# Optimization experiments

Measured on AMD Instinct MI355X. Metric: run time of the kernel, lower is better.

Reference implementation:

```python
import jax, jax.numpy as jnp
import numpy as np

EPS = 1e-5

def layernorm(x, w, b):
    mu = jnp.mean(x, axis=-1, keepdims=True)
    var = jnp.mean((x - mu) ** 2, axis=-1, keepdims=True)
    return (x - mu) / jnp.sqrt(var + EPS) * w + b

def setup_inputs() -> dict:
    key = jax.random.key(0)
    ks = jax.random.split(key, 20)
    N, E, G = 50000, 800000, 512
    IN, OUT, TXT, MAN = 128, 128, 768, 14
    d = {
        "x": jax.random.normal(ks[0], (N, IN), jnp.float32),
        "edge_index": jax.random.randint(ks[1], (2, E), 0, N),
        "batch": jnp.sort(jax.random.randint(ks[2], (N,), 0, G)),
        "batch_size": G,
        "text_embedding": jax.random.normal(ks[3], (G, TXT), jnp.float32),
        "features_embedding": jax.random.normal(ks[4], (G, MAN), jnp.float32),
        # params
        "ln_proj_w": jnp.ones((IN,)), "ln_proj_b": jnp.zeros((IN,)),
        "W_l": jax.random.normal(ks[5], (IN, OUT)) / np.sqrt(IN),
        "b_l": jnp.zeros((OUT,)),
        "W_r": jax.random.normal(ks[6], (IN, OUT)) / np.sqrt(IN),
        "ln_conv_w": jnp.ones((OUT,)), "ln_conv_b": jnp.zeros((OUT,)),
        "gate_w": jax.random.normal(ks[7], (OUT, 1)) / np.sqrt(OUT),
        "gate_b": jnp.zeros((1,)),
        "graph_weight": jnp.asarray(1.0, jnp.float32),
        "msg_W": jax.random.normal(ks[8], (TXT, OUT)) / np.sqrt(TXT),
        "msg_b": jnp.zeros((OUT,)),
        "feat_W": jax.random.normal(ks[9], (MAN, OUT)) / np.sqrt(MAN),
        "feat_b": jnp.zeros((OUT,)),
        "mixed_w": jnp.ones((3 * OUT,)), "mixed_b": jnp.zeros((3 * OUT,)),
        "fc1_W": jax.random.normal(ks[10], (3 * OUT, 1)) / np.sqrt(3 * OUT),
        "fc1_b": jnp.zeros((1,)),
    }
    return d

def reference(x, edge_index, batch, batch_size, text_embedding, features_embedding,
              ln_proj_w, ln_proj_b, W_l, b_l, W_r, ln_conv_w, ln_conv_b,
              gate_w, gate_b, graph_weight, msg_W, msg_b, feat_W, feat_b,
              mixed_w, mixed_b, fc1_W, fc1_b):
    N = x.shape[0]
    src, dst = edge_index[0], edge_index[1]
    # project_norm
    h = layernorm(x, ln_proj_w, ln_proj_b)
    # GraphSAGE (SAGEConv, mean aggregation): out = mean_j(h_j) @ W_l + b + h @ W_r
    msgs = h[src]                                   # [E, IN] gather
    agg = jax.ops.segment_sum(msgs, dst, num_segments=N)
    deg = jax.ops.segment_sum(jnp.ones((src.shape[0],), h.dtype), dst, num_segments=N)
    mean_nb = agg / jnp.maximum(deg, 1.0)[:, None]
    h = mean_nb @ W_l + b_l + h @ W_r
    # layernorm + gelu (HomogeneousGraphConvolution)
    h = jax.nn.gelu(layernorm(h, ln_conv_w, ln_conv_b), approximate=False)
    # AttentionalAggregation: scatter-softmax over `batch`
    gate = (h @ gate_w + gate_b)[:, 0]              # [N]
    seg_max = jax.ops.segment_max(gate, batch, num_segments=batch_size)
    seg_max = jnp.where(jnp.isfinite(seg_max), seg_max, 0.0)
    e = jnp.exp(gate - seg_max[batch])
    denom = jax.ops.segment_sum(e, batch, num_segments=batch_size)
    attn = (e / denom[batch])[:, None]              # [N,1]
    graph_embedding = jax.ops.segment_sum(attn * h, batch, num_segments=batch_size)
    # dropout is identity in eval mode
    weighted = graph_weight * graph_embedding
    msg_emb = jax.nn.gelu(text_embedding @ msg_W + msg_b, approximate=False)
    feat_emb = jax.nn.gelu(features_embedding @ feat_W + feat_b, approximate=False)
    emb = jnp.concatenate([weighted, msg_emb, feat_emb], axis=1)
    emb = layernorm(emb, mixed_w, mixed_b)
    logits = emb @ fc1_W + fc1_b
    return (logits, graph_embedding, attn)
```

## Files before the change

### kernel.cpp

```cpp
#include <hip/hip_runtime.h>


typedef unsigned short ushort_t;
typedef __attribute__((ext_vector_type(8))) short bf16x8;
typedef __attribute__((ext_vector_type(4))) float floatx4;

__device__ __forceinline__ float b2f(ushort_t u) {
    union { unsigned int i; float f; } v; v.i = ((unsigned int)u) << 16; return v.f;
}
__device__ __forceinline__ ushort_t f2b(float f) {
    union { float f; unsigned int i; } v; v.f = f;
    unsigned int x = v.i;
    return (ushort_t)((x + 0x7FFFu + ((x >> 16) & 1u)) >> 16);
}
__device__ __forceinline__ float gelu_f(float x) {
    return 0.5f * x * (1.0f + erff(x * 0.70710678118654752440f));
}
__device__ __forceinline__ float waveReduceSum(float v) {
#pragma unroll
    for (int o = 32; o; o >>= 1) v += __shfl_xor(v, o, 64);
    return v;
}
__device__ __forceinline__ int waveReduceSumI(int v) {
#pragma unroll
    for (int o = 32; o; o >>= 1) v += __shfl_xor(v, o, 64);
    return v;
}
__device__ __forceinline__ float waveReduceMax(float v) {
#pragma unroll
    for (int o = 32; o; o >>= 1) v = fmaxf(v, __shfl_xor(v, o, 64));
    return v;
}
__device__ __forceinline__ int lowerBound(const int* __restrict__ a, int n, int v) {
    int lo = 0, hi = n;
    while (lo < hi) { int mid = (lo + hi) >> 1; if (a[mid] < v) lo = mid + 1; else hi = mid; }
    return lo;
}
__device__ __forceinline__ void acc8(float* a, const bf16x8& r) {
    a[0] += b2f((ushort_t)r[0]); a[1] += b2f((ushort_t)r[1]);
    a[2] += b2f((ushort_t)r[2]); a[3] += b2f((ushort_t)r[3]);
    a[4] += b2f((ushort_t)r[4]); a[5] += b2f((ushort_t)r[5]);
    a[6] += b2f((ushort_t)r[6]); a[7] += b2f((ushort_t)r[7]);
}

__global__ void __launch_bounds__(256) k_cpl(
    const float* __restrict__ x, const float* __restrict__ w, const float* __restrict__ b,
    const float* __restrict__ Wl, const float* __restrict__ Wr,
    const int* __restrict__ ei, int* __restrict__ deg,
    ushort_t* __restrict__ Wt, ushort_t* __restrict__ hb, int N, int E, int ebc) {
    int bid = blockIdx.x;
    if (bid < ebc) {
        int i0 = (bid * 256 + threadIdx.x) * 8;
        const int* dstp = ei + E;
        if (i0 + 7 < E) {
            int4 a = *(const int4*)(dstp + i0);
            int4 c = *(const int4*)(dstp + i0 + 4);
            atomicAdd(&deg[a.x], 1); atomicAdd(&deg[a.y], 1);
            atomicAdd(&deg[a.z], 1); atomicAdd(&deg[a.w], 1);
            atomicAdd(&deg[c.x], 1); atomicAdd(&deg[c.y], 1);
            atomicAdd(&deg[c.z], 1); atomicAdd(&deg[c.w], 1);
        } else {
            int e1 = min(i0 + 8, E);
            for (int i = i0; i < e1; i++) atomicAdd(&deg[dstp[i]], 1);
        }
        return;
    }
    bid -= ebc;
    if (bid < 128) {
        int id = bid * 256 + threadIdx.x;
        int n = id >> 8, k = id & 255;
        float v = (k < 128) ? Wl[k * 128 + n] : Wr[(k - 128) * 128 + n];
        Wt[n * 256 + k] = f2b(v);
        return;
    }
    int lb = bid - 128;
    int row  = lb * 4 + (threadIdx.x >> 6);
    int lane = threadIdx.x & 63;
    if (row >= N) return;
    size_t base = (size_t)row * 128;
    float2 xv = ((const float2*)(x + base))[lane];
    float v0 = xv.x, v1 = xv.y;
    float s  = waveReduceSum(v0 + v1);
    float s2 = waveReduceSum(v0 * v0 + v1 * v1);
    float mu = s * (1.0f / 128.0f);
    float var = s2 * (1.0f / 128.0f) - mu * mu;
    float rstd = 1.0f / sqrtf(var + 1e-5f);
    int d = lane * 2;
    ushort2 ov;
    ov.x = f2b((v0 - mu) * rstd * w[d]     + b[d]);
    ov.y = f2b((v1 - mu) * rstd * w[d + 1] + b[d + 1]);
    ((ushort2*)(hb + base))[lane] = ov;
}

__global__ void __launch_bounds__(256) k_cursor3(
    const int* __restrict__ deg, int* __restrict__ cursor, int* __restrict__ wcur, int N) {
    int c = blockIdx.x, t = threadIdx.x;
    __shared__ int sb[256];
    __shared__ int cw[4];
    int lim = c << 8;
    int part = 0;
    for (int j = t; j < lim; j += 256) part += deg[j];
    part = waveReduceSumI(part);
    int lane = t & 63, wv = t >> 6;
    if (lane == 0) cw[wv] = part;
    int i = (c << 8) + t;
    int v = (i < N) ? deg[i] : 0;
    sb[t] = v;
    __syncthreads();
    for (int o = 1; o < 256; o <<= 1) {
        int a = (t >= o) ? sb[t - o] : 0;
        __syncthreads();
        sb[t] += a;
        __syncthreads();
    }
    int coff = cw[0] + cw[1] + cw[2] + cw[3];
    if (i < N) {
        int cv = sb[t] - v + coff;
        cursor[i] = cv;
        wcur[i]   = cv;
    }
}

__global__ void __launch_bounds__(256) k_place(
    const int* __restrict__ ei, int* __restrict__ wcur, int* __restrict__ nbr, int E) {
    int i0 = (blockIdx.x * 256 + threadIdx.x) * 8;
    if (i0 + 7 < E) {
        int4 s0 = *(const int4*)(ei + i0);
        int4 s1 = *(const int4*)(ei + i0 + 4);
        int4 d0 = *(const int4*)(ei + E + i0);
        int4 d1 = *(const int4*)(ei + E + i0 + 4);
        int p0 = atomicAdd(&wcur[d0.x], 1);
        int p1 = atomicAdd(&wcur[d0.y], 1);
        int p2 = atomicAdd(&wcur[d0.z], 1);
        int p3 = atomicAdd(&wcur[d0.w], 1);
        int p4 = atomicAdd(&wcur[d1.x], 1);
        int p5 = atomicAdd(&wcur[d1.y], 1);
        int p6 = atomicAdd(&wcur[d1.z], 1);
        int p7 = atomicAdd(&wcur[d1.w], 1);
        nbr[p0] = s0.x; nbr[p1] = s0.y; nbr[p2] = s0.z; nbr[p3] = s0.w;
        nbr[p4] = s1.x; nbr[p5] = s1.y; nbr[p6] = s1.z; nbr[p7] = s1.w;
    } else {
        int e1 = min(i0 + 8, E);
        for (int i = i0; i < e1; i++) {
            int s = ei[i], d = ei[E + i];
            nbr[atomicAdd(&wcur[d], 1)] = s;
        }
    }
}

__global__ void __launch_bounds__(256) k_aggemm(
    const ushort_t* __restrict__ hb, const ushort_t* __restrict__ Wt,
    const float* __restrict__ bl, const float* __restrict__ lnw,
    const float* __restrict__ lnb, const float* __restrict__ gw,
    const float* __restrict__ gb, const int* __restrict__ deg,
    const int* __restrict__ cursor, const int* __restrict__ nbr,
    ushort_t* __restrict__ h3b, float* __restrict__ gate, int N) {
    __shared__ ushort_t A[16][264];
    __shared__ float H2[16][132];
    int t = threadIdx.x;
    int row0 = blockIdx.x * 16;
    int w = t >> 6, l = t & 63;
    int sub = l >> 4, li = l & 15;
    {
        int r = w * 4 + sub;
        int node = row0 + r; if (node >= N) node = N - 1;
        bf16x8 hv = *(const bf16x8*)(hb + (size_t)node * 128 + li * 8);
        *(bf16x8*)&A[r][128 + li * 8] = hv;
        int dg = deg[node];
        int st = cursor[node];
        float a[8] = {0.f, 0.f, 0.f, 0.f, 0.f, 0.f, 0.f, 0.f};
        int j = 0;
        for (; j + 8 <= dg; j += 8) {
            int s0 = nbr[st + j],     s1 = nbr[st + j + 1];
            int s2 = nbr[st + j + 2], s3 = nbr[st + j + 3];
            int s4 = nbr[st + j + 4], s5 = nbr[st + j + 5];
            int s6 = nbr[st + j + 6], s7 = nbr[st + j + 7];
            bf16x8 r0 = *(const bf16x8*)(hb + (size_t)s0 * 128 + li * 8);
            bf16x8 r1 = *(const bf16x8*)(hb + (size_t)s1 * 128 + li * 8);
            bf16x8 r2 = *(const bf16x8*)(hb + (size_t)s2 * 128 + li * 8);
            bf16x8 r3 = *(const bf16x8*)(hb + (size_t)s3 * 128 + li * 8);
            bf16x8 r4 = *(const bf16x8*)(hb + (size_t)s4 * 128 + li * 8);
            bf16x8 r5 = *(const bf16x8*)(hb + (size_t)s5 * 128 + li * 8);
            bf16x8 r6 = *(const bf16x8*)(hb + (size_t)s6 * 128 + li * 8);
            bf16x8 r7 = *(const bf16x8*)(hb + (size_t)s7 * 128 + li * 8);
            acc8(a, r0); acc8(a, r1); acc8(a, r2); acc8(a, r3);
            acc8(a, r4); acc8(a, r5); acc8(a, r6); acc8(a, r7);
        }
        for (; j + 4 <= dg; j += 4) {
            int s0 = nbr[st + j],     s1 = nbr[st + j + 1];
            int s2 = nbr[st + j + 2], s3 = nbr[st + j + 3];
            bf16x8 r0 = *(const bf16x8*)(hb + (size_t)s0 * 128 + li * 8);
            bf16x8 r1 = *(const bf16x8*)(hb + (size_t)s1 * 128 + li * 8);
            bf16x8 r2 = *(const bf16x8*)(hb + (size_t)s2 * 128 + li * 8);
            bf16x8 r3 = *(const bf16x8*)(hb + (size_t)s3 * 128 + li * 8);
            acc8(a, r0); acc8(a, r1); acc8(a, r2); acc8(a, r3);
        }
        for (; j < dg; j++) {
            int s = nbr[st + j];
            bf16x8 r0 = *(const bf16x8*)(hb + (size_t)s * 128 + li * 8);
            acc8(a, r0);
        }
        float inv = 1.0f / fmaxf((float)dg, 1.0f);
        bf16x8 ov;
        ov[0] = (short)f2b(a[0] * inv); ov[1] = (short)f2b(a[1] * inv);
        ov[2] = (short)f2b(a[2] * inv); ov[3] = (short)f2b(a[3] * inv);
        ov[4] = (short)f2b(a[4] * inv); ov[5] = (short)f2b(a[5] * inv);
        ov[6] = (short)f2b(a[6] * inv); ov[7] = (short)f2b(a[7] * inv);
        *(bf16x8*)&A[r][li * 8] = ov;
    }
    __syncthreads();
    int m16 = l & 15, quad = l >> 4;
    int n0 = w * 32 + m16;
    int n1 = n0 + 16;
    floatx4 acc0 = {0.f, 0.f, 0.f, 0.f}, acc1 = {0.f, 0.f, 0.f, 0.f};
    for (int ks = 0; ks < 256; ks += 32) {
        bf16x8 a  = *(const bf16x8*)&A[m16][ks + quad * 8];
        bf16x8 b0 = *(const bf16x8*)(Wt + (size_t)n0 * 256 + ks + quad * 8);
        bf16x8 b1 = *(const bf16x8*)(Wt + (size_t)n1 * 256 + ks + quad * 8);
        acc0 = __builtin_amdgcn_mfma_f32_16x16x32_bf16(a, b0, acc0, 0, 0, 0);
        acc1 = __builtin_amdgcn_mfma_f32_16x16x32_bf16(a, b1, acc1, 0, 0, 0);
    }
#pragma unroll
    for (int i = 0; i < 4; i++) {
        H2[quad * 4 + i][n0] = acc0[i];
        H2[quad * 4 + i][n1] = acc1[i];
    }
    __syncthreads();
    int d = l * 2;
    float bb0 = bl[d],  bb1 = bl[d + 1];
    float lw0 = lnw[d], lw1 = lnw[d + 1];
    float lb0 = lnb[d], lb1 = lnb[d + 1];
    float gw0 = gw[d],  gw1 = gw[d + 1];
    float gbias = gb[0];
#pragma unroll
    for (int rr = 0; rr < 4; rr++) {
        int r = w * 4 + rr;
        int row = row0 + r;
        if (row >= N) break;
        float v0 = H2[r][d] + bb0, v1 = H2[r][d + 1] + bb1;
        float s  = waveReduceSum(v0 + v1);
        float s2 = waveReduceSum(v0 * v0 + v1 * v1);
        float mu = s * (1.f / 128.f);
        float var = s2 * (1.f / 128.f) - mu * mu;
        float rstd = 1.0f / sqrtf(var + 1e-5f);
        float g0 = gelu_f((v0 - mu) * rstd * lw0 + lb0);
        float g1 = gelu_f((v1 - mu) * rstd * lw1 + lb1);
        float gp = waveReduceSum(g0 * gw0 + g1 * gw1);
        ushort2 ov; ov.x = f2b(g0); ov.y = f2b(g1);
        ((ushort2*)(h3b + (size_t)row * 128))[l] = ov;
        if (l == 0) gate[row] = gp + gbias;
    }
}

__global__ void __launch_bounds__(128) k_attntail(
    const float* __restrict__ gate, const ushort_t* __restrict__ h3b,
    const int* __restrict__ batch,
    const float* __restrict__ text, const float* __restrict__ feats,
    const float* __restrict__ msgW, const float* __restrict__ msgb,
    const float* __restrict__ featW, const float* __restrict__ featb,
    const float* __restrict__ gwt, const float* __restrict__ mixw,
    const float* __restrict__ mixb, const float* __restrict__ fc1W,
    const float* __restrict__ fc1b,
    float* __restrict__ ge_out, float* __restrict__ attn_out,
    float* __restrict__ logits, int N, int G) {
    int g = blockIdx.x, t = threadIdx.x;
    __shared__ int sbound[2];
    __shared__ float wbuf[2];
    __shared__ float pbuf[128];
    __shared__ float txt[768];
    __shared__ float rbuf[4];
    if (t < 2) sbound[t] = lowerBound(batch, N, g + t);
    for (int i = t; i < 768; i += 128) txt[i] = text[(size_t)g * 768 + i];
    __syncthreads();
    int s0 = sbound[0], s1 = sbound[1];
    int lane = t & 63, wv = t >> 6;
    float acc = 0.f;
    if (s1 > s0) {
        float m = -3.0e38f;
        for (int i = s0 + t; i < s1; i += 128) m = fmaxf(m, gate[i]);
        m = waveReduceMax(m);
        if (lane == 0) wbuf[wv] = m;
        __syncthreads();
        m = fmaxf(wbuf[0], wbuf[1]);
        __syncthreads();
        float dsum = 0.f;
        for (int i = s0 + t; i < s1; i += 128) dsum += expf(gate[i] - m);
        dsum = waveReduceSum(dsum);
        if (lane == 0) wbuf[wv] = dsum;
        __syncthreads();
        float inv = 1.0f / (wbuf[0] + wbuf[1]);
        for (int base = s0; base < s1; base += 128) {
            int n = min(128, s1 - base);
            __syncthreads();
            if (t < n) {
                float p = expf(gate[base + t] - m) * inv;
                pbuf[t] = p;
                attn_out[base + t] = p;
            }
            __syncthreads();
            for (int j = 0; j < n; j++)
                acc += pbuf[j] * b2f(h3b[(size_t)(base + j) * 128 + t]);
        }
    }
    ge_out[(size_t)g * 128 + t] = acc;
    float am = msgb[t];
    for (int k = 0; k < 768; k += 4) {
        float4 a = *(const float4*)&txt[k];
        am += a.x * msgW[(k + 0) * 128 + t] + a.y * msgW[(k + 1) * 128 + t]
            + a.z * msgW[(k + 2) * 128 + t] + a.w * msgW[(k + 3) * 128 + t];
    }
    float me = gelu_f(am);
    float af = featb[t];
#pragma unroll
    for (int k = 0; k < 14; k++) af += feats[g * 14 + k] * featW[k * 128 + t];
    float fe = gelu_f(af);
    float e0 = gwt[0] * acc;
    float ps = e0 + me + fe, ps2 = e0 * e0 + me * me + fe * fe;
    float r1 = waveReduceSum(ps), r2 = waveReduceSum(ps2);
    __syncthreads();
    if (lane == 0) { rbuf[wv] = r1; rbuf[2 + wv] = r2; }
    __syncthreads();
    float S = rbuf[0] + rbuf[1], S2 = rbuf[2] + rbuf[3];
    float mu = S * (1.f / 384.f);
    float var = S2 * (1.f / 384.f) - mu * mu;
    float rstd = 1.0f / sqrtf(var + 1e-5f);
    float n0 = (e0 - mu) * rstd * mixw[t]       + mixb[t];
    float n1 = (me - mu) * rstd * mixw[128 + t] + mixb[128 + t];
    float n2 = (fe - mu) * rstd * mixw[256 + t] + mixb[256 + t];
    float lp = n0 * fc1W[t] + n1 * fc1W[128 + t] + n2 * fc1W[256 + t];
    float r3 = waveReduceSum(lp);
    __syncthreads();
    if (lane == 0) rbuf[wv] = r3;
    __syncthreads();
    if (t == 0) logits[g] = rbuf[0] + rbuf[1] + fc1b[0];
}

extern "C" void kernel_launch(void* const* d_in, const int* in_sizes, int n_in,
                              void* d_out, int out_size, void* d_ws, size_t ws_size,
                              hipStream_t stream) {
    const float* x     = (const float*)d_in[0];
    const int*   ei    = (const int*)d_in[1];
    const int*   batch = (const int*)d_in[2];
    const float* text  = (const float*)d_in[4];
    const float* feats = (const float*)d_in[5];
    const float* lnpw  = (const float*)d_in[6];
    const float* lnpb  = (const float*)d_in[7];
    const float* Wl    = (const float*)d_in[8];
    const float* bl    = (const float*)d_in[9];
    const float* Wr    = (const float*)d_in[10];
    const float* lncw  = (const float*)d_in[11];
    const float* lncb  = (const float*)d_in[12];
    const float* gatew = (const float*)d_in[13];
    const float* gateb = (const float*)d_in[14];
    const float* gwt   = (const float*)d_in[15];
    const float* msgW  = (const float*)d_in[16];
    const float* msgb  = (const float*)d_in[17];
    const float* featW = (const float*)d_in[18];
    const float* featb = (const float*)d_in[19];
    const float* mixw  = (const float*)d_in[20];
    const float* mixb  = (const float*)d_in[21];
    const float* fc1W  = (const float*)d_in[22];
    const float* fc1b  = (const float*)d_in[23];

    int N = in_sizes[0] / 128;
    int E = in_sizes[1] / 2;
    int G = in_sizes[4] / 768;

    char* wp = (char*)d_ws;
    auto alloc = [&](size_t bytes) -> char* {
        char* p = wp; wp += (bytes + 255) & ~(size_t)255; return p;
    };
    ushort_t* hb     = (ushort_t*)alloc((size_t)N * 128 * 2);
    ushort_t* h3b    = (ushort_t*)alloc((size_t)N * 128 * 2);
    ushort_t* Wt     = (ushort_t*)alloc(128 * 256 * 2);
    float*    gate   = (float*)alloc((size_t)N * 4);
    int*      deg    = (int*)alloc((size_t)N * 4);
    int*      cursor = (int*)alloc((size_t)N * 4);
    int*      wcur   = (int*)alloc((size_t)N * 4);
    int*      nbr    = (int*)alloc((size_t)E * 4);

    int nch = (N + 255) / 256;
    int ebc = (E + 2047) / 2048;

    float* logits_out = (float*)d_out;
    float* ge_out     = logits_out + G;
    float* attn_out   = ge_out + (size_t)G * 128;

    hipMemsetAsync(deg, 0, (size_t)N * 4, stream);
    k_cpl      <<<ebc + 128 + (N + 3) / 4, 256, 0, stream>>>(
                                                   x, lnpw, lnpb, Wl, Wr, ei, deg,
                                                   Wt, hb, N, E, ebc);
    k_cursor3  <<<nch,               256, 0, stream>>>(deg, cursor, wcur, N);
    k_place    <<<ebc,               256, 0, stream>>>(ei, wcur, nbr, E);
    k_aggemm   <<<(N + 15) / 16,     256, 0, stream>>>(hb, Wt, bl, lncw, lncb, gatew, gateb,
                                                       deg, cursor, nbr, h3b, gate, N);
    k_attntail <<<G,                 128, 0, stream>>>(gate, h3b, batch, text, feats,
                                                       msgW, msgb, featW, featb, gwt,
                                                       mixw, mixb, fc1W, fc1b,
                                                       ge_out, attn_out, logits_out, N, G);
}
```

Measured before the change: 306.5 us.

## Double attention-tail block width and vectorise bf16 unpack in neighbour aggregation

```diff
diff --git a/kernel.cpp b/kernel.cpp
--- a/kernel.cpp
+++ b/kernel.cpp
@@ -2,11 +2,18 @@
 
 
 typedef unsigned short ushort_t;
+typedef unsigned int uint_t;
 typedef __attribute__((ext_vector_type(8))) short bf16x8;
 typedef __attribute__((ext_vector_type(4))) float floatx4;
+typedef __attribute__((ext_vector_type(2))) float f32x2;
 
 __device__ __forceinline__ float b2f(ushort_t u) {
     union { unsigned int i; float f; } v; v.i = ((unsigned int)u) << 16; return v.f;
+}
+__device__ __forceinline__ f32x2 b2f2(uint_t u) {
+    union { unsigned int i; float f; } lo, hi;
+    lo.i = u << 16; hi.i = u & 0xFFFF0000u;
+    f32x2 r; r.x = lo.f; r.y = hi.f; return r;
 }
 __device__ __forceinline__ ushort_t f2b(float f) {
     union { float f; unsigned int i; } v; v.f = f;
@@ -35,12 +42,6 @@
     int lo = 0, hi = n;
     while (lo < hi) { int mid = (lo + hi) >> 1; if (a[mid] < v) lo = mid + 1; else hi = mid; }
     return lo;
-}
-__device__ __forceinline__ void acc8(float* a, const bf16x8& r) {
-    a[0] += b2f((ushort_t)r[0]); a[1] += b2f((ushort_t)r[1]);
-    a[2] += b2f((ushort_t)r[2]); a[3] += b2f((ushort_t)r[3]);
-    a[4] += b2f((ushort_t)r[4]); a[5] += b2f((ushort_t)r[5]);
-    a[6] += b2f((ushort_t)r[6]); a[7] += b2f((ushort_t)r[7]);
 }
 
 __global__ void __launch_bounds__(256) k_cpl(
@@ -168,44 +169,42 @@
         *(bf16x8*)&A[r][128 + li * 8] = hv;
         int dg = deg[node];
         int st = cursor[node];
-        float a[8] = {0.f, 0.f, 0.f, 0.f, 0.f, 0.f, 0.f, 0.f};
+        f32x2 a0 = {0.f, 0.f}, a1 = {0.f, 0.f}, a2 = {0.f, 0.f}, a3 = {0.f, 0.f};
+        const uint_t* hp = (const uint_t*)hb;
+#define ROWPTR(s) ((const uint4*)(hp + (size_t)(s) * 64 + li * 4))
+#define ACCQ(q) { a0 += b2f2((q).x); a1 += b2f2((q).y); a2 += b2f2((q).z); a3 += b2f2((q).w); }
         int j = 0;
         for (; j + 8 <= dg; j += 8) {
-            int s0 = nbr[st + j],     s1 = nbr[st + j + 1];
-            int s2 = nbr[st + j + 2], s3 = nbr[st + j + 3];
-            int s4 = nbr[st + j + 4], s5 = nbr[st + j + 5];
-            int s6 = nbr[st + j + 6], s7 = nbr[st + j + 7];
-            bf16x8 r0 = *(const bf16x8*)(hb + (size_t)s0 * 128 + li * 8);
-            bf16x8 r1 = *(const bf16x8*)(hb + (size_t)s1 * 128 + li * 8);
-            bf16x8 r2 = *(const bf16x8*)(hb + (size_t)s2 * 128 + li * 8);
-            bf16x8 r3 = *(const bf16x8*)(hb + (size_t)s3 * 128 + li * 8);
-            bf16x8 r4 = *(const bf16x8*)(hb + (size_t)s4 * 128 + li * 8);
-            bf16x8 r5 = *(const bf16x8*)(hb + (size_t)s5 * 128 + li * 8);
-            bf16x8 r6 = *(const bf16x8*)(hb + (size_t)s6 * 128 + li * 8);
-            bf16x8 r7 = *(const bf16x8*)(hb + (size_t)s7 * 128 + li * 8);
-            acc8(a, r0); acc8(a, r1); acc8(a, r2); acc8(a, r3);
-            acc8(a, r4); acc8(a, r5); acc8(a, r6); acc8(a, r7);
+            uint4 q0 = *ROWPTR(nbr[st + j]);
+            uint4 q1 = *ROWPTR(nbr[st + j + 1]);
+            uint4 q2 = *ROWPTR(nbr[st + j + 2]);
+            uint4 q3 = *ROWPTR(nbr[st + j + 3]);
+            uint4 q4 = *ROWPTR(nbr[st + j + 4]);
+            uint4 q5 = *ROWPTR(nbr[st + j + 5]);
+            uint4 q6 = *ROWPTR(nbr[st + j + 6]);
+            uint4 q7 = *ROWPTR(nbr[st + j + 7]);
+            ACCQ(q0); ACCQ(q1); ACCQ(q2); ACCQ(q3);
+            ACCQ(q4); ACCQ(q5); ACCQ(q6); ACCQ(q7);
         }
         for (; j + 4 <= dg; j += 4) {
-            int s0 = nbr[st + j],     s1 = nbr[st + j + 1];
-            int s2 = nbr[st + j + 2], s3 = nbr[st + j + 3];
-            bf16x8 r0 = *(const bf16x8*)(hb + (size_t)s0 * 128 + li * 8);
-            bf16x8 r1 = *(const bf16x8*)(hb + (size_t)s1 * 128 + li * 8);
-            bf16x8 r2 = *(const bf16x8*)(hb + (size_t)s2 * 128 + li * 8);
-            bf16x8 r3 = *(const bf16x8*)(hb + (size_t)s3 * 128 + li * 8);
-            acc8(a, r0); acc8(a, r1); acc8(a, r2); acc8(a, r3);
+            uint4 q0 = *ROWPTR(nbr[st + j]);
+            uint4 q1 = *ROWPTR(nbr[st + j + 1]);
+            uint4 q2 = *ROWPTR(nbr[st + j + 2]);
+            uint4 q3 = *ROWPTR(nbr[st + j + 3]);
+            ACCQ(q0); ACCQ(q1); ACCQ(q2); ACCQ(q3);
         }
         for (; j < dg; j++) {
-            int s = nbr[st + j];
-            bf16x8 r0 = *(const bf16x8*)(hb + (size_t)s * 128 + li * 8);
-            acc8(a, r0);
-        }
+            uint4 q0 = *ROWPTR(nbr[st + j]);
+            ACCQ(q0);
+        }
+#undef ROWPTR
+#undef ACCQ
         float inv = 1.0f / fmaxf((float)dg, 1.0f);
         bf16x8 ov;
-        ov[0] = (short)f2b(a[0] * inv); ov[1] = (short)f2b(a[1] * inv);
-        ov[2] = (short)f2b(a[2] * inv); ov[3] = (short)f2b(a[3] * inv);
-        ov[4] = (short)f2b(a[4] * inv); ov[5] = (short)f2b(a[5] * inv);
-        ov[6] = (short)f2b(a[6] * inv); ov[7] = (short)f2b(a[7] * inv);
+        ov[0] = (short)f2b(a0.x * inv); ov[1] = (short)f2b(a0.y * inv);
+        ov[2] = (short)f2b(a1.x * inv); ov[3] = (short)f2b(a1.y * inv);
+        ov[4] = (short)f2b(a2.x * inv); ov[5] = (short)f2b(a2.y * inv);
+        ov[6] = (short)f2b(a3.x * inv); ov[7] = (short)f2b(a3.y * inv);
         *(bf16x8*)&A[r][li * 8] = ov;
     }
     __syncthreads();
@@ -252,7 +251,7 @@
     }
 }
 
-__global__ void __launch_bounds__(128) k_attntail(
+__global__ void __launch_bounds__(256) k_attntail(
     const float* __restrict__ gate, const ushort_t* __restrict__ h3b,
     const int* __restrict__ batch,
     const float* __restrict__ text, const float* __restrict__ feats,
@@ -263,52 +262,63 @@
     const float* __restrict__ fc1b,
     float* __restrict__ ge_out, float* __restrict__ attn_out,
     float* __restrict__ logits, int N, int G) {
-    int g = blockIdx.x, t = threadIdx.x;
+    int g = blockIdx.x, tid = threadIdx.x;
+    int h = tid >> 7, t = tid & 127;
     __shared__ int sbound[2];
-    __shared__ float wbuf[2];
-    __shared__ float pbuf[128];
+    __shared__ float wbuf[4];
+    __shared__ float pbuf[256];
     __shared__ float txt[768];
-    __shared__ float rbuf[4];
-    if (t < 2) sbound[t] = lowerBound(batch, N, g + t);
-    for (int i = t; i < 768; i += 128) txt[i] = text[(size_t)g * 768 + i];
+    __shared__ float accb[256];
+    __shared__ float rbuf[8];
+    if (tid < 2) sbound[tid] = lowerBound(batch, N, g + tid);
+    for (int i = tid; i < 768; i += 256) txt[i] = text[(size_t)g * 768 + i];
     __syncthreads();
     int s0 = sbound[0], s1 = sbound[1];
-    int lane = t & 63, wv = t >> 6;
+    int lane = tid & 63, wv = tid >> 6;
     float acc = 0.f;
     if (s1 > s0) {
         float m = -3.0e38f;
-        for (int i = s0 + t; i < s1; i += 128) m = fmaxf(m, gate[i]);
+        for (int i = s0 + tid; i < s1; i += 256) m = fmaxf(m, gate[i]);
         m = waveReduceMax(m);
         if (lane == 0) wbuf[wv] = m;
         __syncthreads();
-        m = fmaxf(wbuf[0], wbuf[1]);
+        m = fmaxf(fmaxf(wbuf[0], wbuf[1]), fmaxf(wbuf[2], wbuf[3]));
         __syncthreads();
         float dsum = 0.f;
-        for (int i = s0 + t; i < s1; i += 128) dsum += expf(gate[i] - m);
+        for (int i = s0 + tid; i < s1; i += 256) dsum += expf(gate[i] - m);
         dsum = waveReduceSum(dsum);
         if (lane == 0) wbuf[wv] = dsum;
         __syncthreads();
-        float inv = 1.0f / (wbuf[0] + wbuf[1]);
-        for (int base = s0; base < s1; base += 128) {
-            int n = min(128, s1 - base);
+        float inv = 1.0f / (wbuf[0] + wbuf[1] + wbuf[2] + wbuf[3]);
+        for (int base = s0; base < s1; base += 256) {
+            int n = min(256, s1 - base);
             __syncthreads();
-            if (t < n) {
-                float p = expf(gate[base + t] - m) * inv;
-                pbuf[t] = p;
-                attn_out[base + t] = p;
+            if (tid < n) {
+                float p = expf(gate[base + tid] - m) * inv;
+                pbuf[tid] = p;
+                attn_out[base + tid] = p;
             }
             __syncthreads();
-            for (int j = 0; j < n; j++)
+            int j1 = min(n, h * 128 + 128);
+            for (int j = h * 128; j < j1; j++)
                 acc += pbuf[j] * b2f(h3b[(size_t)(base + j) * 128 + t]);
         }
     }
-    ge_out[(size_t)g * 128 + t] = acc;
-    float am = msgb[t];
-    for (int k = 0; k < 768; k += 4) {
+    accb[tid] = acc;
+    __syncthreads();
+    acc = accb[t] + accb[t + 128];
+    if (h == 0) ge_out[(size_t)g * 128 + t] = acc;
+    float am = (h == 0) ? msgb[t] : 0.f;
+    int k0 = h * 384;
+    for (int k = k0; k < k0 + 384; k += 4) {
         float4 a = *(const float4*)&txt[k];
         am += a.x * msgW[(k + 0) * 128 + t] + a.y * msgW[(k + 1) * 128 + t]
             + a.z * msgW[(k + 2) * 128 + t] + a.w * msgW[(k + 3) * 128 + t];
     }
+    __syncthreads();
+    accb[tid] = am;
+    __syncthreads();
+    am = accb[t] + accb[t + 128];
     float me = gelu_f(am);
     float af = featb[t];
 #pragma unroll
@@ -318,9 +328,10 @@
     float ps = e0 + me + fe, ps2 = e0 * e0 + me * me + fe * fe;
     float r1 = waveReduceSum(ps), r2 = waveReduceSum(ps2);
     __syncthreads();
-    if (lane == 0) { rbuf[wv] = r1; rbuf[2 + wv] = r2; }
-    __syncthreads();
-    float S = rbuf[0] + rbuf[1], S2 = rbuf[2] + rbuf[3];
+    if (lane == 0) { rbuf[wv] = r1; rbuf[4 + wv] = r2; }
+    __syncthreads();
+    float S  = (rbuf[0] + rbuf[1] + rbuf[2] + rbuf[3]) * 0.5f;
+    float S2 = (rbuf[4] + rbuf[5] + rbuf[6] + rbuf[7]) * 0.5f;
     float mu = S * (1.f / 384.f);
     float var = S2 * (1.f / 384.f) - mu * mu;
     float rstd = 1.0f / sqrtf(var + 1e-5f);
@@ -332,7 +343,8 @@
     __syncthreads();
     if (lane == 0) rbuf[wv] = r3;
     __syncthreads();
-    if (t == 0) logits[g] = rbuf[0] + rbuf[1] + fc1b[0];
+    if (tid == 0)
+        logits[g] = (rbuf[0] + rbuf[1] + rbuf[2] + rbuf[3]) * 0.5f + fc1b[0];
 }
 
 extern "C" void kernel_launch(void* const* d_in, const int* in_sizes, int n_in,
@@ -394,7 +406,7 @@
     k_place    <<<ebc,               256, 0, stream>>>(ei, wcur, nbr, E);
     k_aggemm   <<<(N + 15) / 16,     256, 0, stream>>>(hb, Wt, bl, lncw, lncb, gatew, gateb,
                                                        deg, cursor, nbr, h3b, gate, N);
-    k_attntail <<<G,                 128, 0, stream>>>(gate, h3b, batch, text, feats,
+    k_attntail <<<G,                 256, 0, stream>>>(gate, h3b, batch, text, feats,
                                                        msgW, msgb, featW, featb, gwt,
                                                        mixw, mixb, fc1W, fc1b,
                                                        ge_out, attn_out, logits_out, N, G);
```

Measured after the change: 322.4 us. +5.2%, slower.

## Fuse degree count, layernorm, scan and CSR placement into one cooperative kernel

Applied to the files above, without the earlier changes.

```diff
diff --git a/kernel.cpp b/kernel.cpp
--- a/kernel.cpp
+++ b/kernel.cpp
@@ -1,9 +1,15 @@
 #include <hip/hip_runtime.h>
+#include <hip/hip_cooperative_groups.h>
+
+namespace cg = cooperative_groups;
 
 
 typedef unsigned short ushort_t;
 typedef __attribute__((ext_vector_type(8))) short bf16x8;
 typedef __attribute__((ext_vector_type(4))) float floatx4;
+
+#define MEGA_BLOCKS 1024
+#define CNT_BLOCKS  256
 
 __device__ __forceinline__ float b2f(ushort_t u) {
     union { unsigned int i; float f; } v; v.i = ((unsigned int)u) << 16; return v.f;
@@ -43,107 +49,122 @@
     a[6] += b2f((ushort_t)r[6]); a[7] += b2f((ushort_t)r[7]);
 }
 
-__global__ void __launch_bounds__(256) k_cpl(
+__global__ void __launch_bounds__(256, 4) k_mega(
     const float* __restrict__ x, const float* __restrict__ w, const float* __restrict__ b,
     const float* __restrict__ Wl, const float* __restrict__ Wr,
     const int* __restrict__ ei, int* __restrict__ deg,
-    ushort_t* __restrict__ Wt, ushort_t* __restrict__ hb, int N, int E, int ebc) {
-    int bid = blockIdx.x;
-    if (bid < ebc) {
-        int i0 = (bid * 256 + threadIdx.x) * 8;
+    int* __restrict__ cursor, int* __restrict__ wcur, int* __restrict__ nbr,
+    ushort_t* __restrict__ Wt, ushort_t* __restrict__ hb,
+    int N, int E, int nch) {
+    cg::grid_group grid = cg::this_grid();
+    __shared__ int sb[256];
+    __shared__ int cw[4];
+    int bid = blockIdx.x, t = threadIdx.x;
+    int nblk = (int)gridDim.x;
+
+    for (int i = bid * 256 + t; i < N; i += nblk * 256) deg[i] = 0;
+    __threadfence();
+    grid.sync();
+
+    if (bid < CNT_BLOCKS) {
         const int* dstp = ei + E;
-        if (i0 + 7 < E) {
-            int4 a = *(const int4*)(dstp + i0);
-            int4 c = *(const int4*)(dstp + i0 + 4);
-            atomicAdd(&deg[a.x], 1); atomicAdd(&deg[a.y], 1);
-            atomicAdd(&deg[a.z], 1); atomicAdd(&deg[a.w], 1);
-            atomicAdd(&deg[c.x], 1); atomicAdd(&deg[c.y], 1);
-            atomicAdd(&deg[c.z], 1); atomicAdd(&deg[c.w], 1);
-        } else {
-            int e1 = min(i0 + 8, E);
-            for (int i = i0; i < e1; i++) atomicAdd(&deg[dstp[i]], 1);
-        }
-        return;
-    }
-    bid -= ebc;
-    if (bid < 128) {
-        int id = bid * 256 + threadIdx.x;
+        int stride = CNT_BLOCKS * 256 * 8;
+        for (int i0 = (bid * 256 + t) * 8; i0 < E; i0 += stride) {
+            if (i0 + 7 < E) {
+                int4 a = *(const int4*)(dstp + i0);
+                int4 c = *(const int4*)(dstp + i0 + 4);
+                atomicAdd(&deg[a.x], 1); atomicAdd(&deg[a.y], 1);
+                atomicAdd(&deg[a.z], 1); atomicAdd(&deg[a.w], 1);
+                atomicAdd(&deg[c.x], 1); atomicAdd(&deg[c.y], 1);
+                atomicAdd(&deg[c.z], 1); atomicAdd(&deg[c.w], 1);
+            } else {
+                int e1 = min(i0 + 8, E);
+                for (int i = i0; i < e1; i++) atomicAdd(&deg[dstp[i]], 1);
+            }
+        }
+    } else if (bid < CNT_BLOCKS + 128) {
+        int id = (bid - CNT_BLOCKS) * 256 + t;
         int n = id >> 8, k = id & 255;
         float v = (k < 128) ? Wl[k * 128 + n] : Wr[(k - 128) * 128 + n];
         Wt[n * 256 + k] = f2b(v);
-        return;
-    }
-    int lb = bid - 128;
-    int row  = lb * 4 + (threadIdx.x >> 6);
-    int lane = threadIdx.x & 63;
-    if (row >= N) return;
-    size_t base = (size_t)row * 128;
-    float2 xv = ((const float2*)(x + base))[lane];
-    float v0 = xv.x, v1 = xv.y;
-    float s  = waveReduceSum(v0 + v1);
-    float s2 = waveReduceSum(v0 * v0 + v1 * v1);
-    float mu = s * (1.0f / 128.0f);
-    float var = s2 * (1.0f / 128.0f) - mu * mu;
-    float rstd = 1.0f / sqrtf(var + 1e-5f);
-    int d = lane * 2;
-    ushort2 ov;
-    ov.x = f2b((v0 - mu) * rstd * w[d]     + b[d]);
-    ov.y = f2b((v1 - mu) * rstd * w[d + 1] + b[d + 1]);
-    ((ushort2*)(hb + base))[lane] = ov;
-}
-
-__global__ void __launch_bounds__(256) k_cursor3(
-    const int* __restrict__ deg, int* __restrict__ cursor, int* __restrict__ wcur, int N) {
-    int c = blockIdx.x, t = threadIdx.x;
-    __shared__ int sb[256];
-    __shared__ int cw[4];
-    int lim = c << 8;
-    int part = 0;
-    for (int j = t; j < lim; j += 256) part += deg[j];
-    part = waveReduceSumI(part);
-    int lane = t & 63, wv = t >> 6;
-    if (lane == 0) cw[wv] = part;
-    int i = (c << 8) + t;
-    int v = (i < N) ? deg[i] : 0;
-    sb[t] = v;
-    __syncthreads();
-    for (int o = 1; o < 256; o <<= 1) {
-        int a = (t >= o) ? sb[t - o] : 0;
+    } else {
+        int lnb = bid - (CNT_BLOCKS + 128);
+        int nLN = nblk - (CNT_BLOCKS + 128);
+        int lane = t & 63;
+        for (int base = lnb * 4; base < N; base += nLN * 4) {
+            int row = base + (t >> 6);
+            if (row >= N) continue;
+            size_t rb = (size_t)row * 128;
+            float2 xv = ((const float2*)(x + rb))[lane];
+            float v0 = xv.x, v1 = xv.y;
+            float s  = waveReduceSum(v0 + v1);
+            float s2 = waveReduceSum(v0 * v0 + v1 * v1);
+            float mu = s * (1.0f / 128.0f);
+            float var = s2 * (1.0f / 128.0f) - mu * mu;
+            float rstd = 1.0f / sqrtf(var + 1e-5f);
+            int d = lane * 2;
+            ushort2 ov;
+            ov.x = f2b((v0 - mu) * rstd * w[d]     + b[d]);
+            ov.y = f2b((v1 - mu) * rstd * w[d + 1] + b[d + 1]);
+            ((ushort2*)(hb + rb))[lane] = ov;
+        }
+    }
+    __threadfence();
+    grid.sync();
+
+    if (bid < nch) {
+        int c = bid;
+        int lim = c << 8;
+        int part = 0;
+        for (int j = t; j < lim; j += 256) part += deg[j];
+        part = waveReduceSumI(part);
+        int lane = t & 63, wv = t >> 6;
+        if (lane == 0) cw[wv] = part;
+        int i = (c << 8) + t;
+        int v = (i < N) ? deg[i] : 0;
+        sb[t] = v;
         __syncthreads();
-        sb[t] += a;
-        __syncthreads();
-    }
-    int coff = cw[0] + cw[1] + cw[2] + cw[3];
-    if (i < N) {
-        int cv = sb[t] - v + coff;
-        cursor[i] = cv;
-        wcur[i]   = cv;
-    }
-}
-
-__global__ void __launch_bounds__(256) k_place(
-    const int* __restrict__ ei, int* __restrict__ wcur, int* __restrict__ nbr, int E) {
-    int i0 = (blockIdx.x * 256 + threadIdx.x) * 8;
-    if (i0 + 7 < E) {
-        int4 s0 = *(const int4*)(ei + i0);
-        int4 s1 = *(const int4*)(ei + i0 + 4);
-        int4 d0 = *(const int4*)(ei + E + i0);
-        int4 d1 = *(const int4*)(ei + E + i0 + 4);
-        int p0 = atomicAdd(&wcur[d0.x], 1);
-        int p1 = atomicAdd(&wcur[d0.y], 1);
-        int p2 = atomicAdd(&wcur[d0.z], 1);
-        int p3 = atomicAdd(&wcur[d0.w], 1);
-        int p4 = atomicAdd(&wcur[d1.x], 1);
-        int p5 = atomicAdd(&wcur[d1.y], 1);
-        int p6 = atomicAdd(&wcur[d1.z], 1);
-        int p7 = atomicAdd(&wcur[d1.w], 1);
-        nbr[p0] = s0.x; nbr[p1] = s0.y; nbr[p2] = s0.z; nbr[p3] = s0.w;
-        nbr[p4] = s1.x; nbr[p5] = s1.y; nbr[p6] = s1.z; nbr[p7] = s1.w;
-    } else {
-        int e1 = min(i0 + 8, E);
-        for (int i = i0; i < e1; i++) {
-            int s = ei[i], d = ei[E + i];
-            nbr[atomicAdd(&wcur[d], 1)] = s;
+        for (int o = 1; o < 256; o <<= 1) {
+            int a = (t >= o) ? sb[t - o] : 0;
+            __syncthreads();
+            sb[t] += a;
+            __syncthreads();
+        }
+        int coff = cw[0] + cw[1] + cw[2] + cw[3];
+        if (i < N) {
+            int cv = sb[t] - v + coff;
+            cursor[i] = cv;
+            wcur[i]   = cv;
+        }
+    }
+    __threadfence();
+    grid.sync();
+
+    {
+        int stride = nblk * 256 * 8;
+        for (int i0 = (bid * 256 + t) * 8; i0 < E; i0 += stride) {
+            if (i0 + 7 < E) {
+                int4 s0 = *(const int4*)(ei + i0);
+                int4 s1 = *(const int4*)(ei + i0 + 4);
+                int4 d0 = *(const int4*)(ei + E + i0);
+                int4 d1 = *(const int4*)(ei + E + i0 + 4);
+                int p0 = atomicAdd(&wcur[d0.x], 1);
+                int p1 = atomicAdd(&wcur[d0.y], 1);
+                int p2 = atomicAdd(&wcur[d0.z], 1);
+                int p3 = atomicAdd(&wcur[d0.w], 1);
+                int p4 = atomicAdd(&wcur[d1.x], 1);
+                int p5 = atomicAdd(&wcur[d1.y], 1);
+                int p6 = atomicAdd(&wcur[d1.z], 1);
+                int p7 = atomicAdd(&wcur[d1.w], 1);
+                nbr[p0] = s0.x; nbr[p1] = s0.y; nbr[p2] = s0.z; nbr[p3] = s0.w;
+                nbr[p4] = s1.x; nbr[p5] = s1.y; nbr[p6] = s1.z; nbr[p7] = s1.w;
+            } else {
+                int e1 = min(i0 + 8, E);
+                for (int i = i0; i < e1; i++) {
+                    int s = ei[i], d = ei[E + i];
+                    nbr[atomicAdd(&wcur[d], 1)] = s;
+                }
+            }
         }
     }
 }
@@ -380,22 +401,23 @@
     int*      nbr    = (int*)alloc((size_t)E * 4);
 
     int nch = (N + 255) / 256;
-    int ebc = (E + 2047) / 2048;
 
     float* logits_out = (float*)d_out;
     float* ge_out     = logits_out + G;
     float* attn_out   = ge_out + (size_t)G * 128;
 
-    hipMemsetAsync(deg, 0, (size_t)N * 4, stream);
-    k_cpl      <<<ebc + 128 + (N + 3) / 4, 256, 0, stream>>>(
-                                                   x, lnpw, lnpb, Wl, Wr, ei, deg,
-                                                   Wt, hb, N, E, ebc);
-    k_cursor3  <<<nch,               256, 0, stream>>>(deg, cursor, wcur, N);
-    k_place    <<<ebc,               256, 0, stream>>>(ei, wcur, nbr, E);
-    k_aggemm   <<<(N + 15) / 16,     256, 0, stream>>>(hb, Wt, bl, lncw, lncb, gatew, gateb,
-                                                       deg, cursor, nbr, h3b, gate, N);
-    k_attntail <<<G,                 128, 0, stream>>>(gate, h3b, batch, text, feats,
-                                                       msgW, msgb, featW, featb, gwt,
-                                                       mixw, mixb, fc1W, fc1b,
-                                                       ge_out, attn_out, logits_out, N, G);
-}
+    void* kargs[] = {
+        (void*)&x, (void*)&lnpw, (void*)&lnpb, (void*)&Wl, (void*)&Wr,
+        (void*)&ei, (void*)&deg, (void*)&cursor, (void*)&wcur, (void*)&nbr,
+        (void*)&Wt, (void*)&hb, (void*)&N, (void*)&E, (void*)&nch
+    };
+    hipLaunchCooperativeKernel((const void*)k_mega, dim3(MEGA_BLOCKS), dim3(256),
+                               kargs, 0, stream);
+
+    k_aggemm   <<<(N + 15) / 16, 256, 0, stream>>>(hb, Wt, bl, lncw, lncb, gatew, gateb,
+                                                   deg, cursor, nbr, h3b, gate, N);
+    k_attntail <<<G,             128, 0, stream>>>(gate, h3b, batch, text, feats,
+                                                   msgW, msgb, featW, featb, gwt,
+                                                   mixw, mixb, fc1W, fc1b,
+                                                   ge_out, attn_out, logits_out, N, G);
+}
```

Result: slower. 813.3 us (+165.3%).
